# Kernel optimization log

Measured on AMD Instinct MI355X. Metric: run time of the kernel, lower is better.

Reference implementation:

```python
import jax, jax.numpy as jnp
import numpy as np


def hard_sigmoid(x):
    # Keras hard_sigmoid: clip(0.2*x + 0.5, 0, 1)
    return jnp.clip(x * 0.2 + 0.5, 0.0, 1.0)


def conv2d_same(x, w):
    # x: [B,H,W,Cin], w: [kh,kw,Cin,Cout]
    return jax.lax.conv_general_dilated(
        x, w, window_strides=(1, 1), padding='SAME',
        dimension_numbers=('NHWC', 'HWIO', 'NHWC'))


def convlstm2d(x, Wx, Wh, b):
    # x: [B,T,H,W,Cin]; Wx: [k,k,Cin,4*Cout]; Wh: [k,k,Cout,4*Cout]; b: [4*Cout]
    B, T, H, W, _ = x.shape
    Cout = Wh.shape[2]
    h0 = jnp.zeros((B, H, W, Cout), x.dtype)
    c0 = jnp.zeros((B, H, W, Cout), x.dtype)

    def step(carry, xt):
        h, c = carry
        z = conv2d_same(xt, Wx) + conv2d_same(h, Wh) + b
        i, f, g, o = jnp.split(z, 4, axis=-1)  # Keras gate order i,f,c,o
        c = hard_sigmoid(f) * c + hard_sigmoid(i) * jnp.tanh(g)
        h = hard_sigmoid(o) * jnp.tanh(c)
        return (h, c), h

    _, hs = jax.lax.scan(step, (h0, c0), jnp.moveaxis(x, 1, 0))
    return jnp.moveaxis(hs, 0, 1)  # [B,T,H,W,Cout]


def bn_inference(x, gamma, beta, mean, var, eps=1e-3):
    # Keras BatchNormalization default eps=1e-3, inference mode (training=False)
    return (x - mean) * jax.lax.rsqrt(var + eps) * gamma + beta


def upsample_2x2(x):
    # UpSampling3D(size=(1,2,2)) on [B,T,H,W,C]
    return jnp.repeat(jnp.repeat(x, 2, axis=2), 2, axis=3)


def deconv_block(x, Wx, Wh, b, g, be, mm, mv):
    return upsample_2x2(bn_inference(convlstm2d(x, Wx, Wh, b), g, be, mm, mv))


def setup_inputs() -> dict:
    key = jax.random.key(0)
    ks = jax.random.split(key, 32)
    B, T, H, W = 2, 8, 16, 16
    Cin = 192
    chans = [128, 64, 32]
    K = 3
    d = {'x': jax.random.normal(ks[0], (B, T, H, W, Cin), jnp.float32)}
    ci = Cin
    ki = 1
    for l, co in enumerate(chans, start=1):
        d[f'Wx{l}'] = jax.random.normal(ks[ki], (K, K, ci, 4 * co), jnp.float32) * 0.05; ki += 1
        d[f'Wh{l}'] = jax.random.normal(ks[ki], (K, K, co, 4 * co), jnp.float32) * 0.05; ki += 1
        d[f'b{l}'] = jnp.zeros((4 * co,), jnp.float32)
        d[f'g{l}'] = jax.random.uniform(ks[ki], (co,), jnp.float32) + 0.5; ki += 1
        d[f'be{l}'] = jax.random.normal(ks[ki], (co,), jnp.float32) * 0.1; ki += 1
        d[f'mm{l}'] = jax.random.normal(ks[ki], (co,), jnp.float32) * 0.1; ki += 1
        d[f'mv{l}'] = jax.random.uniform(ks[ki], (co,), jnp.float32) + 0.5; ki += 1
        ci = co
    return d


def reference(x, Wx1, Wh1, b1, g1, be1, mm1, mv1,
              Wx2, Wh2, b2, g2, be2, mm2, mv2,
              Wx3, Wh3, b3, g3, be3, mm3, mv3):
    x = deconv_block(x, Wx1, Wh1, b1, g1, be1, mm1, mv1)  # [2,8,32,32,128]
    x = deconv_block(x, Wx2, Wh2, b2, g2, be2, mm2, mv2)  # [2,8,64,64,64]
    x = deconv_block(x, Wx3, Wh3, b3, g3, be3, mm3, mv3)  # [2,8,128,128,32]
    return x
```

## Files before the change

### kernel.cpp

```cpp
#include <hip/hip_runtime.h>
#include <math.h>

#define BATCH 2
#define TSTEPS 8

typedef __attribute__((ext_vector_type(8))) short s16x8;
typedef __attribute__((ext_vector_type(4))) float f32x4;

__device__ __forceinline__ float hsig(float v){ return fminf(fmaxf(0.2f*v+0.5f,0.f),1.f); }
__device__ __forceinline__ ushort f2bf(float f){
    uint u = __builtin_bit_cast(uint, f);
    u = (u + 0x7FFFu + ((u >> 16) & 1u)) >> 16;
    return (ushort)u;
}
__device__ __forceinline__ uint pack2bf(float lo, float hi){
    return (uint)f2bf(lo) | ((uint)f2bf(hi) << 16);
}

template<int KCH, int Co>
__device__ __forceinline__ void packw(const float* __restrict__ W, ushort* __restrict__ dst, int d){
    int j = d & 7, lane = (d >> 3) & 63;
    int q = lane >> 4, l = lane & 15;
    int rest = d >> 9;
    int c = rest % KCH, t_n = rest / KCH;
    int k = c*32 + q*8 + j;
    int np = t_n*16 + l;
    int g = np & 3, co = np >> 2;
    dst[d] = f2bf(W[(size_t)k*(4*Co) + g*Co + co]);
}

#define SZ_X    786432
#define SZ_WX1  884736
#define SZ_WH1  589824
#define SZ_WX2  294912
#define SZ_WH2  147456
#define SZ_WX3  73728
#define SZ_WH3  36864
#define SZ_PREP (SZ_X+SZ_WX1+SZ_WH1+SZ_WX2+SZ_WH2+SZ_WX3+SZ_WH3)

struct Params {
    const float *x, *Wx1, *Wh1, *b1, *g1, *be1, *mm1, *mv1;
    const float *Wx2, *Wh2, *b2, *g2, *be2, *mm2, *mv2;
    const float *Wx3, *Wh3, *b3, *g3, *be3, *mm3, *mv3;
    float *c1, *c2, *c3;
    char  *zbase;
    ushort *xpad, *x2pad, *x3pad, *h1A, *h1B, *h2A, *h2B, *h3A, *h3B;
    ushort *Wxp1, *Wxp2, *Wxp3, *Whp1, *Whp2, *Whp3;
    float *out;
};

__device__ __forceinline__ void prep_elem(int i, const Params& p){
    if (i < SZ_X){
        int c = i % 192; int r = i / 192;
        int xx = r % 16; r /= 16; int yy = r % 16; int bt = r / 16;
        p.xpad[((size_t)bt*18*18 + (yy+1)*18 + (xx+1))*192 + c] = f2bf(p.x[i]);
        return;
    } i -= SZ_X;
    if (i < SZ_WX1){ packw<54,128>(p.Wx1, p.Wxp1, i); return; } i -= SZ_WX1;
    if (i < SZ_WH1){ packw<36,128>(p.Wh1, p.Whp1, i); return; } i -= SZ_WH1;
    if (i < SZ_WX2){ packw<36, 64>(p.Wx2, p.Wxp2, i); return; } i -= SZ_WX2;
    if (i < SZ_WH2){ packw<18, 64>(p.Wh2, p.Whp2, i); return; } i -= SZ_WH2;
    if (i < SZ_WX3){ packw<18, 32>(p.Wx3, p.Wxp3, i); return; } i -= SZ_WX3;
    if (i < SZ_WH3){ packw< 9, 32>(p.Wh3, p.Whp3, i); }
}

__global__ __launch_bounds__(256) void prep_kernel_g(Params p){
    int i = blockIdx.x*256 + threadIdx.x;
    if (i < SZ_PREP) prep_elem(i, p);
}

template<int CI, int CO, int H, int W, int OUT_BF16>
__device__ __forceinline__ void fused_role(char* smem, int lbid, int t, int first,
    const ushort* __restrict__ Apad, const ushort* __restrict__ Wxpk,
    const ushort* __restrict__ hprev, const ushort* __restrict__ Whpk,
    const float* __restrict__ bias,
    ushort* __restrict__ hnew, float* __restrict__ cst,
    const float* __restrict__ gamma, const float* __restrict__ beta,
    const float* __restrict__ mmean, const float* __restrict__ mvar,
    void* __restrict__ outp)
{
    constexpr int W_T = (W < 32) ? W : 32;
    constexpr int PR = (32/W_T) + 2, PPX = W_T + 2;
    constexpr int PCI = CI + 8, PCO = CO + 8;
    constexpr int KX = 9*CI/32, CPTX = CI/32;
    constexpr int KH = 9*CO/32, CPTH = CO/32;
    constexpr int NJX = (KX + 3)/4, NJH = (KH + 3)/4;
    constexpr int HW = H*W, HP = H+2, WP = W+2;
    constexpr int CH8X = CI/8, CH8H = CO/8;
    constexpr int TOTX = PR*PPX*CH8X, TOTH = PR*PPX*CH8H;
    constexpr int PT = (BATCH*HW)/32;

    ushort* patch = (ushort*)smem;
    float* Zs = (float*)smem;
    float* Hs = (float*)(smem + 18432);

    const int tid = threadIdx.x, lane = tid & 63, wave = tid >> 6;
    const int quad = lane >> 4, l16 = lane & 15;
    const int pxt = lbid % PT, colIdx = lbid / PT;
    const int m0 = pxt * 32;
    const int b2 = m0 / HW, rem = m0 - b2*HW;
    const int y0 = rem / W, x0 = rem - (rem/W)*W;
    const int co0 = colIdx * 8;
    const int tn0 = colIdx * 2;
    const int bt = b2*TSTEPS + t;

    f32x4 acc[2][2] = {};

    {
        const ushort* gsrc = Apad + (size_t)bt*HP*WP*CI;
        for (int c = tid; c < TOTX; c += 256){
            int pix = c / CH8X, ch = c - pix*CH8X;
            int prow = pix / PPX, ppx = pix - prow*PPX;
            *(uint4*)&patch[pix*PCI + ch*8] =
                *(const uint4*)(gsrc + ((size_t)(y0+prow)*WP + (x0+ppx))*CI + ch*8);
        }
        __syncthreads();

        const ushort* bp0 = Wxpk + ((size_t)tn0*KX*64 + lane)*8;
        const ushort* bp1 = Wxpk + ((size_t)(tn0+1)*KX*64 + lane)*8;
        int labase[2];
        #pragma unroll
        for (int s = 0; s < 2; ++s){
            int pp = s*16 + l16;
            int rp = pp / W_T, xp = pp - rp*W_T;
            labase[s] = (rp*PPX + xp)*PCI + quad*8;
        }
        const int nj = (KX - wave + 3) >> 2;
        #pragma unroll
        for (int j = 0; j < NJX; ++j){
            if (j < nj){
                const int it = wave + 4*j;
                const int tap = it / CPTX, ci0 = (it - tap*CPTX)*32;
                const int kh = tap/3, kw = tap - (tap/3)*3;
                const int off = (kh*PPX + kw)*PCI + ci0;
                s16x8 b0 = *(const s16x8*)(bp0 + (size_t)it*512);
                s16x8 b1 = *(const s16x8*)(bp1 + (size_t)it*512);
                s16x8 a0 = *(const s16x8*)&patch[labase[0] + off];
                s16x8 a1 = *(const s16x8*)&patch[labase[1] + off];
                acc[0][0] = __builtin_amdgcn_mfma_f32_16x16x32_bf16(a0, b0, acc[0][0], 0,0,0);
                acc[0][1] = __builtin_amdgcn_mfma_f32_16x16x32_bf16(a0, b1, acc[0][1], 0,0,0);
                acc[1][0] = __builtin_amdgcn_mfma_f32_16x16x32_bf16(a1, b0, acc[1][0], 0,0,0);
                acc[1][1] = __builtin_amdgcn_mfma_f32_16x16x32_bf16(a1, b1, acc[1][1], 0,0,0);
            }
        }
        __syncthreads();
    }

    if (!first){
        const ushort* gsrc = hprev + (size_t)b2*HP*WP*CO;
        for (int c = tid; c < TOTH; c += 256){
            int pix = c / CH8H, ch = c - pix*CH8H;
            int prow = pix / PPX, ppx = pix - prow*PPX;
            *(uint4*)&patch[pix*PCO + ch*8] =
                *(const uint4*)(gsrc + ((size_t)(y0+prow)*WP + (x0+ppx))*CO + ch*8);
        }
        __syncthreads();

        const ushort* bp0 = Whpk + ((size_t)tn0*KH*64 + lane)*8;
        const ushort* bp1 = Whpk + ((size_t)(tn0+1)*KH*64 + lane)*8;
        int labase[2];
        #pragma unroll
        for (int s = 0; s < 2; ++s){
            int pp = s*16 + l16;
            int rp = pp / W_T, xp = pp - rp*W_T;
            labase[s] = (rp*PPX + xp)*PCO + quad*8;
        }
        const int nj = (KH - wave + 3) >> 2;
        #pragma unroll
        for (int j = 0; j < NJH; ++j){
            if (j < nj){
                const int it = wave + 4*j;
                const int tap = it / CPTH, ci0 = (it - tap*CPTH)*32;
                const int kh = tap/3, kw = tap - (tap/3)*3;
                const int off = (kh*PPX + kw)*PCO + ci0;
                s16x8 b0 = *(const s16x8*)(bp0 + (size_t)it*512);
                s16x8 b1 = *(const s16x8*)(bp1 + (size_t)it*512);
                s16x8 a0 = *(const s16x8*)&patch[labase[0] + off];
                s16x8 a1 = *(const s16x8*)&patch[labase[1] + off];
                acc[0][0] = __builtin_amdgcn_mfma_f32_16x16x32_bf16(a0, b0, acc[0][0], 0,0,0);
                acc[0][1] = __builtin_amdgcn_mfma_f32_16x16x32_bf16(a0, b1, acc[0][1], 0,0,0);
                acc[1][0] = __builtin_amdgcn_mfma_f32_16x16x32_bf16(a1, b0, acc[1][0], 0,0,0);
                acc[1][1] = __builtin_amdgcn_mfma_f32_16x16x32_bf16(a1, b1, acc[1][1], 0,0,0);
            }
        }
        __syncthreads();
    }

    #pragma unroll
    for (int s = 0; s < 2; ++s)
        #pragma unroll
        for (int nt = 0; nt < 2; ++nt)
            #pragma unroll
            for (int r = 0; r < 4; ++r)
                Zs[(wave*32 + s*16 + quad*4 + r)*36 + nt*16 + l16] = acc[s][nt][r];
    __syncthreads();

    {
        const int px = tid >> 3, coin = tid & 7;
        const int m = m0 + px;
        const int rr = m - b2*HW;
        const int co = co0 + coin;
        float zi = 0.f, zf = 0.f, zg = 0.f, zo = 0.f;
        #pragma unroll
        for (int w = 0; w < 4; ++w){
            const float4 s = *(const float4*)&Zs[(w*32 + px)*36 + coin*4];
            zi += s.x; zf += s.y; zg += s.z; zo += s.w;
        }
        zi += bias[0*CO + co]; zf += bias[1*CO + co];
        zg += bias[2*CO + co]; zo += bias[3*CO + co];
        const float iv = hsig(zi), fv = hsig(zf);
        const float gv = tanhf(zg), ov = hsig(zo);
        const float cold = first ? 0.f : cst[(size_t)m*CO + co];
        const float cn = fv*cold + iv*gv;
        cst[(size_t)m*CO + co] = cn;
        const float h = ov * tanhf(cn);
        const int y = rr / W, x = rr - (rr/W)*W;
        hnew[((size_t)b2*HP*WP + (y+1)*WP + (x+1))*CO + co] = f2bf(h);
        Hs[px*8 + coin] = (h - mmean[co])*rsqrtf(mvar[co]+1e-3f)*gamma[co] + beta[co];
    }
    __syncthreads();

    if (OUT_BF16){
        if (tid < 128){
            const int px = tid >> 2, q = tid & 3;
            const int ypos = q >> 1, xpos = q & 1;
            const int m = m0 + px;
            const int rr = m - b2*HW;
            const int y = rr / W, x = rr - (rr/W)*W;
            const float* hs = &Hs[px*8];
            uint4 v;
            v.x = pack2bf(hs[0], hs[1]); v.y = pack2bf(hs[2], hs[3]);
            v.z = pack2bf(hs[4], hs[5]); v.w = pack2bf(hs[6], hs[7]);
            ushort* o = (ushort*)outp;
            const size_t opix = ((size_t)bt*(2*H+2) + 2*y+1+ypos)*(size_t)(2*W+2) + 2*x+1+xpos;
            *(uint4*)&o[opix*CO + co0] = v;
        }
    } else {
        const int px = tid >> 3, q = (tid >> 1) & 3, half = tid & 1;
        const int ypos = q >> 1, xpos = q & 1;
        const int m = m0 + px;
        const int rr = m - b2*HW;
        const int y = rr / W, x = rr - (rr/W)*W;
        float4 v = *(const float4*)&Hs[px*8 + half*4];
        float* o = (float*)outp;
        const size_t opix = ((size_t)bt*(2*H) + 2*y+ypos)*(size_t)(2*W) + 2*x+xpos;
        *(float4*)&o[opix*CO + co0 + half*4] = v;
    }
}

__global__ __launch_bounds__(256) void mega(Params p, int e1, int e2,
                                            int t1, int t2, int t3)
{
    __shared__ __align__(16) char smem[28800];
    const int bid = blockIdx.x;
    if (bid < e1){
        const ushort* hp = (t1 & 1) ? p.h1B : p.h1A;
        ushort*       hn = (t1 & 1) ? p.h1A : p.h1B;
        fused_role<192,128,16,16,1>(smem, bid, t1, t1==0,
            p.xpad, p.Wxp1, hp, p.Whp1, p.b1, hn, p.c1,
            p.g1, p.be1, p.mm1, p.mv1, p.x2pad);
    } else if (bid < e2){
        const ushort* hp = (t2 & 1) ? p.h2B : p.h2A;
        ushort*       hn = (t2 & 1) ? p.h2A : p.h2B;
        fused_role<128,64,32,32,1>(smem, bid - e1, t2, t2==0,
            p.x2pad, p.Wxp2, hp, p.Whp2, p.b2, hn, p.c2,
            p.g2, p.be2, p.mm2, p.mv2, p.x3pad);
    } else {
        const ushort* hp = (t3 & 1) ? p.h3B : p.h3A;
        ushort*       hn = (t3 & 1) ? p.h3A : p.h3B;
        fused_role<64,32,64,64,0>(smem, bid - e2, t3, t3==0,
            p.x3pad, p.Wxp3, hp, p.Whp3, p.b3, hn, p.c3,
            p.g3, p.be3, p.mm3, p.mv3, p.out);
    }
}

extern "C" void kernel_launch(void* const* d_in, const int* in_sizes, int n_in,
                              void* d_out, int out_size, void* d_ws, size_t ws_size,
                              hipStream_t stream) {
    Params p;
    p.x   = (const float*)d_in[0];
    p.Wx1 = (const float*)d_in[1];  p.Wh1 = (const float*)d_in[2];
    p.b1  = (const float*)d_in[3];  p.g1  = (const float*)d_in[4];
    p.be1 = (const float*)d_in[5];  p.mm1 = (const float*)d_in[6];
    p.mv1 = (const float*)d_in[7];
    p.Wx2 = (const float*)d_in[8];  p.Wh2 = (const float*)d_in[9];
    p.b2  = (const float*)d_in[10]; p.g2  = (const float*)d_in[11];
    p.be2 = (const float*)d_in[12]; p.mm2 = (const float*)d_in[13];
    p.mv2 = (const float*)d_in[14];
    p.Wx3 = (const float*)d_in[15]; p.Wh3 = (const float*)d_in[16];
    p.b3  = (const float*)d_in[17]; p.g3  = (const float*)d_in[18];
    p.be3 = (const float*)d_in[19]; p.mm3 = (const float*)d_in[20];
    p.mv3 = (const float*)d_in[21];

    char* ws = (char*)d_ws;
    size_t off = 0;
    auto alloc = [&](size_t bytes) { char* q = ws + off; off += (bytes + 255) & ~(size_t)255; return q; };

    p.c1  = (float*)alloc(65536ull * 4);
    p.c2  = (float*)alloc(131072ull * 4);
    p.c3  = (float*)alloc(262144ull * 4);

    p.zbase = alloc(17685504ull);
    p.xpad  = (ushort*)p.zbase;
    p.x2pad = p.xpad  + 995328;
    p.x3pad = p.x2pad + 2367488;
    p.h1A   = p.x3pad + 4460544;
    p.h1B   = p.h1A + 82944;
    p.h2A   = p.h1B + 82944;
    p.h2B   = p.h2A + 147968;
    p.h3A   = p.h2B + 147968;
    p.h3B   = p.h3A + 278784;

    p.Wxp1 = (ushort*)alloc(884736ull * 2);
    p.Wxp2 = (ushort*)alloc(294912ull * 2);
    p.Wxp3 = (ushort*)alloc(73728ull * 2);
    p.Whp1 = (ushort*)alloc(589824ull * 2);
    p.Whp2 = (ushort*)alloc(147456ull * 2);
    p.Whp3 = (ushort*)alloc(36864ull * 2);

    p.out = (float*)d_out;

    hipMemsetAsync(p.zbase, 0, 17685504ull, stream);

    prep_kernel_g<<<(SZ_PREP + 255) / 256, 256, 0, stream>>>(p);

    for (int j = 0; j <= 9; ++j){
        const int aS1 = (j <= 7);
        const int aS2 = (j >= 1 && j <= 8);
        const int aS3 = (j >= 2);
        const int e1 = aS1 ? 256 : 0;
        const int e2 = e1 + (aS2 ? 512 : 0);
        const int e3 = e2 + (aS3 ? 1024 : 0);
        const int t1 = aS1 ? j     : 0;
        const int t2 = aS2 ? j - 1 : 0;
        const int t3 = aS3 ? j - 2 : 0;
        mega<<<dim3(e3), 256, 0, stream>>>(p, e1, e2, t1, t2, t3);
    }
}
```

Before: 258.2 us.

## Compute two column blocks per workgroup for layers 2-3, padding K to multiples of four

Layers 2 and 3 now have each workgroup compute two 8-channel output column blocks (NCPB=2). Each A-fragment read from LDS feeds twice as many MFMAs, and the im2col patch load is amortised over twice the output columns, which halves the grid size for those layers. Packed weights are zero-padded along K to a multiple of four so the per-wave guard on the K loop can be dropped. Costs are more accumulator registers, larger shared memory (38912 bytes) and fewer blocks per launch, which could reduce occupancy and parallelism.

```diff
diff --git a/kernel.cpp b/kernel.cpp
--- a/kernel.cpp
+++ b/kernel.cpp
@@ -17,12 +17,13 @@
     return (uint)f2bf(lo) | ((uint)f2bf(hi) << 16);
 }
 
-template<int KCH, int Co>
+template<int KCH, int KCHP, int Co>
 __device__ __forceinline__ void packw(const float* __restrict__ W, ushort* __restrict__ dst, int d){
     int j = d & 7, lane = (d >> 3) & 63;
     int q = lane >> 4, l = lane & 15;
     int rest = d >> 9;
-    int c = rest % KCH, t_n = rest / KCH;
+    int c = rest % KCHP, t_n = rest / KCHP;
+    if (c >= KCH){ dst[d] = 0; return; }
     int k = c*32 + q*8 + j;
     int np = t_n*16 + l;
     int g = np & 3, co = np >> 2;
@@ -30,12 +31,12 @@
 }
 
 #define SZ_X    786432
-#define SZ_WX1  884736
+#define SZ_WX1  917504
 #define SZ_WH1  589824
 #define SZ_WX2  294912
-#define SZ_WH2  147456
-#define SZ_WX3  73728
-#define SZ_WH3  36864
+#define SZ_WH2  163840
+#define SZ_WX3   81920
+#define SZ_WH3   49152
 #define SZ_PREP (SZ_X+SZ_WX1+SZ_WH1+SZ_WX2+SZ_WH2+SZ_WX3+SZ_WH3)
 
 struct Params {
@@ -56,12 +57,12 @@
         p.xpad[((size_t)bt*18*18 + (yy+1)*18 + (xx+1))*192 + c] = f2bf(p.x[i]);
         return;
     } i -= SZ_X;
-    if (i < SZ_WX1){ packw<54,128>(p.Wx1, p.Wxp1, i); return; } i -= SZ_WX1;
-    if (i < SZ_WH1){ packw<36,128>(p.Wh1, p.Whp1, i); return; } i -= SZ_WH1;
-    if (i < SZ_WX2){ packw<36, 64>(p.Wx2, p.Wxp2, i); return; } i -= SZ_WX2;
-    if (i < SZ_WH2){ packw<18, 64>(p.Wh2, p.Whp2, i); return; } i -= SZ_WH2;
-    if (i < SZ_WX3){ packw<18, 32>(p.Wx3, p.Wxp3, i); return; } i -= SZ_WX3;
-    if (i < SZ_WH3){ packw< 9, 32>(p.Wh3, p.Whp3, i); }
+    if (i < SZ_WX1){ packw<54,56,128>(p.Wx1, p.Wxp1, i); return; } i -= SZ_WX1;
+    if (i < SZ_WH1){ packw<36,36,128>(p.Wh1, p.Whp1, i); return; } i -= SZ_WH1;
+    if (i < SZ_WX2){ packw<36,36, 64>(p.Wx2, p.Wxp2, i); return; } i -= SZ_WX2;
+    if (i < SZ_WH2){ packw<18,20, 64>(p.Wh2, p.Whp2, i); return; } i -= SZ_WH2;
+    if (i < SZ_WX3){ packw<18,20, 32>(p.Wx3, p.Wxp3, i); return; } i -= SZ_WX3;
+    if (i < SZ_WH3){ packw< 9,12, 32>(p.Wh3, p.Whp3, i); }
 }
 
 __global__ __launch_bounds__(256) void prep_kernel_g(Params p){
@@ -69,7 +70,7 @@
     if (i < SZ_PREP) prep_elem(i, p);
 }
 
-template<int CI, int CO, int H, int W, int OUT_BF16>
+template<int CI, int CO, int H, int W, int OUT_BF16, int NCPB>
 __device__ __forceinline__ void fused_role(char* smem, int lbid, int t, int first,
     const ushort* __restrict__ Apad, const ushort* __restrict__ Wxpk,
     const ushort* __restrict__ hprev, const ushort* __restrict__ Whpk,
@@ -84,7 +85,8 @@
     constexpr int PCI = CI + 8, PCO = CO + 8;
     constexpr int KX = 9*CI/32, CPTX = CI/32;
     constexpr int KH = 9*CO/32, CPTH = CO/32;
-    constexpr int NJX = (KX + 3)/4, NJH = (KH + 3)/4;
+    constexpr int KXP = (KX + 3) & ~3, KHP = (KH + 3) & ~3;
+    constexpr int NJX = KXP/4, NJH = KHP/4;
     constexpr int HW = H*W, HP = H+2, WP = W+2;
     constexpr int CH8X = CI/8, CH8H = CO/8;
     constexpr int TOTX = PR*PPX*CH8X, TOTH = PR*PPX*CH8H;
@@ -92,19 +94,26 @@
 
     ushort* patch = (ushort*)smem;
     float* Zs = (float*)smem;
-    float* Hs = (float*)(smem + 18432);
+    float* Hs = (float*)(smem + NCPB*18432);
 
     const int tid = threadIdx.x, lane = tid & 63, wave = tid >> 6;
     const int quad = lane >> 4, l16 = lane & 15;
-    const int pxt = lbid % PT, colIdx = lbid / PT;
+    const int pxt = lbid % PT, colB = lbid / PT;
     const int m0 = pxt * 32;
     const int b2 = m0 / HW, rem = m0 - b2*HW;
     const int y0 = rem / W, x0 = rem - (rem/W)*W;
-    const int co0 = colIdx * 8;
-    const int tn0 = colIdx * 2;
     const int bt = b2*TSTEPS + t;
 
-    f32x4 acc[2][2] = {};
+    f32x4 acc[NCPB][2][2] = {};
+
+    int labaseX[2], labaseH[2];
+    #pragma unroll
+    for (int s = 0; s < 2; ++s){
+        int pp = s*16 + l16;
+        int rp = pp / W_T, xp = pp - rp*W_T;
+        labaseX[s] = (rp*PPX + xp)*PCI + quad*8;
+        labaseH[s] = (rp*PPX + xp)*PCO + quad*8;
+    }
 
     {
         const ushort* gsrc = Apad + (size_t)bt*HP*WP*CI;
@@ -116,31 +125,30 @@
         }
         __syncthreads();
 
-        const ushort* bp0 = Wxpk + ((size_t)tn0*KX*64 + lane)*8;
-        const ushort* bp1 = Wxpk + ((size_t)(tn0+1)*KX*64 + lane)*8;
-        int labase[2];
-        #pragma unroll
-        for (int s = 0; s < 2; ++s){
-            int pp = s*16 + l16;
-            int rp = pp / W_T, xp = pp - rp*W_T;
-            labase[s] = (rp*PPX + xp)*PCI + quad*8;
-        }
-        const int nj = (KX - wave + 3) >> 2;
+        const ushort* bp[NCPB][2];
+        #pragma unroll
+        for (int cc = 0; cc < NCPB; ++cc){
+            const int tn = (colB*NCPB + cc)*2;
+            bp[cc][0] = Wxpk + ((size_t)tn*KXP*64 + lane)*8;
+            bp[cc][1] = Wxpk + ((size_t)(tn+1)*KXP*64 + lane)*8;
+        }
         #pragma unroll
         for (int j = 0; j < NJX; ++j){
-            if (j < nj){
-                const int it = wave + 4*j;
-                const int tap = it / CPTX, ci0 = (it - tap*CPTX)*32;
-                const int kh = tap/3, kw = tap - (tap/3)*3;
-                const int off = (kh*PPX + kw)*PCI + ci0;
-                s16x8 b0 = *(const s16x8*)(bp0 + (size_t)it*512);
-                s16x8 b1 = *(const s16x8*)(bp1 + (size_t)it*512);
-                s16x8 a0 = *(const s16x8*)&patch[labase[0] + off];
-                s16x8 a1 = *(const s16x8*)&patch[labase[1] + off];
-                acc[0][0] = __builtin_amdgcn_mfma_f32_16x16x32_bf16(a0, b0, acc[0][0], 0,0,0);
-                acc[0][1] = __builtin_amdgcn_mfma_f32_16x16x32_bf16(a0, b1, acc[0][1], 0,0,0);
-                acc[1][0] = __builtin_amdgcn_mfma_f32_16x16x32_bf16(a1, b0, acc[1][0], 0,0,0);
-                acc[1][1] = __builtin_amdgcn_mfma_f32_16x16x32_bf16(a1, b1, acc[1][1], 0,0,0);
+            const int it = wave + 4*j;
+            const int itA = (it < KX) ? it : 0;
+            const int tap = itA / CPTX, ci0 = (itA - tap*CPTX)*32;
+            const int kh = tap/3, kw = tap - (tap/3)*3;
+            const int off = (kh*PPX + kw)*PCI + ci0;
+            s16x8 a0 = *(const s16x8*)&patch[labaseX[0] + off];
+            s16x8 a1 = *(const s16x8*)&patch[labaseX[1] + off];
+            #pragma unroll
+            for (int cc = 0; cc < NCPB; ++cc){
+                s16x8 b0 = *(const s16x8*)(bp[cc][0] + (size_t)it*512);
+                s16x8 b1 = *(const s16x8*)(bp[cc][1] + (size_t)it*512);
+                acc[cc][0][0] = __builtin_amdgcn_mfma_f32_16x16x32_bf16(a0, b0, acc[cc][0][0], 0,0,0);
+                acc[cc][0][1] = __builtin_amdgcn_mfma_f32_16x16x32_bf16(a0, b1, acc[cc][0][1], 0,0,0);
+                acc[cc][1][0] = __builtin_amdgcn_mfma_f32_16x16x32_bf16(a1, b0, acc[cc][1][0], 0,0,0);
+                acc[cc][1][1] = __builtin_amdgcn_mfma_f32_16x16x32_bf16(a1, b1, acc[cc][1][1], 0,0,0);
             }
         }
         __syncthreads();
@@ -156,54 +164,56 @@
         }
         __syncthreads();
 
-        const ushort* bp0 = Whpk + ((size_t)tn0*KH*64 + lane)*8;
-        const ushort* bp1 = Whpk + ((size_t)(tn0+1)*KH*64 + lane)*8;
-        int labase[2];
-        #pragma unroll
-        for (int s = 0; s < 2; ++s){
-            int pp = s*16 + l16;
-            int rp = pp / W_T, xp = pp - rp*W_T;
-            labase[s] = (rp*PPX + xp)*PCO + quad*8;
-        }
-        const int nj = (KH - wave + 3) >> 2;
+        const ushort* bp[NCPB][2];
+        #pragma unroll
+        for (int cc = 0; cc < NCPB; ++cc){
+            const int tn = (colB*NCPB + cc)*2;
+            bp[cc][0] = Whpk + ((size_t)tn*KHP*64 + lane)*8;
+            bp[cc][1] = Whpk + ((size_t)(tn+1)*KHP*64 + lane)*8;
+        }
         #pragma unroll
         for (int j = 0; j < NJH; ++j){
-            if (j < nj){
-                const int it = wave + 4*j;
-                const int tap = it / CPTH, ci0 = (it - tap*CPTH)*32;
-                const int kh = tap/3, kw = tap - (tap/3)*3;
-                const int off = (kh*PPX + kw)*PCO + ci0;
-                s16x8 b0 = *(const s16x8*)(bp0 + (size_t)it*512);
-                s16x8 b1 = *(const s16x8*)(bp1 + (size_t)it*512);
-                s16x8 a0 = *(const s16x8*)&patch[labase[0] + off];
-                s16x8 a1 = *(const s16x8*)&patch[labase[1] + off];
-                acc[0][0] = __builtin_amdgcn_mfma_f32_16x16x32_bf16(a0, b0, acc[0][0], 0,0,0);
-                acc[0][1] = __builtin_amdgcn_mfma_f32_16x16x32_bf16(a0, b1, acc[0][1], 0,0,0);
-                acc[1][0] = __builtin_amdgcn_mfma_f32_16x16x32_bf16(a1, b0, acc[1][0], 0,0,0);
-                acc[1][1] = __builtin_amdgcn_mfma_f32_16x16x32_bf16(a1, b1, acc[1][1], 0,0,0);
+            const int it = wave + 4*j;
+            const int itA = (it < KH) ? it : 0;
+            const int tap = itA / CPTH, ci0 = (itA - tap*CPTH)*32;
+            const int kh = tap/3, kw = tap - (tap/3)*3;
+            const int off = (kh*PPX + kw)*PCO + ci0;
+            s16x8 a0 = *(const s16x8*)&patch[labaseH[0] + off];
+            s16x8 a1 = *(const s16x8*)&patch[labaseH[1] + off];
+            #pragma unroll
+            for (int cc = 0; cc < NCPB; ++cc){
+                s16x8 b0 = *(const s16x8*)(bp[cc][0] + (size_t)it*512);
+                s16x8 b1 = *(const s16x8*)(bp[cc][1] + (size_t)it*512);
+                acc[cc][0][0] = __builtin_amdgcn_mfma_f32_16x16x32_bf16(a0, b0, acc[cc][0][0], 0,0,0);
+                acc[cc][0][1] = __builtin_amdgcn_mfma_f32_16x16x32_bf16(a0, b1, acc[cc][0][1], 0,0,0);
+                acc[cc][1][0] = __builtin_amdgcn_mfma_f32_16x16x32_bf16(a1, b0, acc[cc][1][0], 0,0,0);
+                acc[cc][1][1] = __builtin_amdgcn_mfma_f32_16x16x32_bf16(a1, b1, acc[cc][1][1], 0,0,0);
             }
         }
         __syncthreads();
     }
 
     #pragma unroll
-    for (int s = 0; s < 2; ++s)
-        #pragma unroll
-        for (int nt = 0; nt < 2; ++nt)
+    for (int cc = 0; cc < NCPB; ++cc)
+        #pragma unroll
+        for (int s = 0; s < 2; ++s)
             #pragma unroll
-            for (int r = 0; r < 4; ++r)
-                Zs[(wave*32 + s*16 + quad*4 + r)*36 + nt*16 + l16] = acc[s][nt][r];
+            for (int nt = 0; nt < 2; ++nt)
+                #pragma unroll
+                for (int r = 0; r < 4; ++r)
+                    Zs[cc*4608 + (wave*32 + s*16 + quad*4 + r)*36 + nt*16 + l16] = acc[cc][s][nt][r];
     __syncthreads();
 
-    {
+    #pragma unroll
+    for (int cc = 0; cc < NCPB; ++cc){
         const int px = tid >> 3, coin = tid & 7;
         const int m = m0 + px;
         const int rr = m - b2*HW;
-        const int co = co0 + coin;
+        const int co = (colB*NCPB + cc)*8 + coin;
         float zi = 0.f, zf = 0.f, zg = 0.f, zo = 0.f;
         #pragma unroll
         for (int w = 0; w < 4; ++w){
-            const float4 s = *(const float4*)&Zs[(w*32 + px)*36 + coin*4];
+            const float4 s = *(const float4*)&Zs[cc*4608 + (w*32 + px)*36 + coin*4];
             zi += s.x; zf += s.y; zg += s.z; zo += s.w;
         }
         zi += bias[0*CO + co]; zf += bias[1*CO + co];
@@ -216,59 +226,63 @@
         const float h = ov * tanhf(cn);
         const int y = rr / W, x = rr - (rr/W)*W;
         hnew[((size_t)b2*HP*WP + (y+1)*WP + (x+1))*CO + co] = f2bf(h);
-        Hs[px*8 + coin] = (h - mmean[co])*rsqrtf(mvar[co]+1e-3f)*gamma[co] + beta[co];
+        Hs[cc*256 + px*8 + coin] = (h - mmean[co])*rsqrtf(mvar[co]+1e-3f)*gamma[co] + beta[co];
     }
     __syncthreads();
 
-    if (OUT_BF16){
-        if (tid < 128){
-            const int px = tid >> 2, q = tid & 3;
+    #pragma unroll
+    for (int cc = 0; cc < NCPB; ++cc){
+        const int co0 = (colB*NCPB + cc)*8;
+        if (OUT_BF16){
+            if (tid < 128){
+                const int px = tid >> 2, q = tid & 3;
+                const int ypos = q >> 1, xpos = q & 1;
+                const int m = m0 + px;
+                const int rr = m - b2*HW;
+                const int y = rr / W, x = rr - (rr/W)*W;
+                const float* hs = &Hs[cc*256 + px*8];
+                uint4 v;
+                v.x = pack2bf(hs[0], hs[1]); v.y = pack2bf(hs[2], hs[3]);
+                v.z = pack2bf(hs[4], hs[5]); v.w = pack2bf(hs[6], hs[7]);
+                ushort* o = (ushort*)outp;
+                const size_t opix = ((size_t)bt*(2*H+2) + 2*y+1+ypos)*(size_t)(2*W+2) + 2*x+1+xpos;
+                *(uint4*)&o[opix*CO + co0] = v;
+            }
+        } else {
+            const int px = tid >> 3, q = (tid >> 1) & 3, half = tid & 1;
             const int ypos = q >> 1, xpos = q & 1;
             const int m = m0 + px;
             const int rr = m - b2*HW;
             const int y = rr / W, x = rr - (rr/W)*W;
-            const float* hs = &Hs[px*8];
-            uint4 v;
-            v.x = pack2bf(hs[0], hs[1]); v.y = pack2bf(hs[2], hs[3]);
-            v.z = pack2bf(hs[4], hs[5]); v.w = pack2bf(hs[6], hs[7]);
-            ushort* o = (ushort*)outp;
-            const size_t opix = ((size_t)bt*(2*H+2) + 2*y+1+ypos)*(size_t)(2*W+2) + 2*x+1+xpos;
-            *(uint4*)&o[opix*CO + co0] = v;
-        }
-    } else {
-        const int px = tid >> 3, q = (tid >> 1) & 3, half = tid & 1;
-        const int ypos = q >> 1, xpos = q & 1;
-        const int m = m0 + px;
-        const int rr = m - b2*HW;
-        const int y = rr / W, x = rr - (rr/W)*W;
-        float4 v = *(const float4*)&Hs[px*8 + half*4];
-        float* o = (float*)outp;
-        const size_t opix = ((size_t)bt*(2*H) + 2*y+ypos)*(size_t)(2*W) + 2*x+xpos;
-        *(float4*)&o[opix*CO + co0 + half*4] = v;
-    }
-}
-
-__global__ __launch_bounds__(256) void mega(Params p, int e1, int e2,
-                                            int t1, int t2, int t3)
+            float4 v = *(const float4*)&Hs[cc*256 + px*8 + half*4];
+            float* o = (float*)outp;
+            const size_t opix = ((size_t)bt*(2*H) + 2*y+ypos)*(size_t)(2*W) + 2*x+xpos;
+            *(float4*)&o[opix*CO + co0 + half*4] = v;
+        }
+    }
+}
+
+__global__ __launch_bounds__(256, 4) void mega(Params p, int e1, int e2,
+                                               int t1, int t2, int t3)
 {
-    __shared__ __align__(16) char smem[28800];
+    __shared__ __align__(16) char smem[38912];
     const int bid = blockIdx.x;
     if (bid < e1){
         const ushort* hp = (t1 & 1) ? p.h1B : p.h1A;
         ushort*       hn = (t1 & 1) ? p.h1A : p.h1B;
-        fused_role<192,128,16,16,1>(smem, bid, t1, t1==0,
+        fused_role<192,128,16,16,1,1>(smem, bid, t1, t1==0,
             p.xpad, p.Wxp1, hp, p.Whp1, p.b1, hn, p.c1,
             p.g1, p.be1, p.mm1, p.mv1, p.x2pad);
     } else if (bid < e2){
         const ushort* hp = (t2 & 1) ? p.h2B : p.h2A;
         ushort*       hn = (t2 & 1) ? p.h2A : p.h2B;
-        fused_role<128,64,32,32,1>(smem, bid - e1, t2, t2==0,
+        fused_role<128,64,32,32,1,2>(smem, bid - e1, t2, t2==0,
             p.x2pad, p.Wxp2, hp, p.Whp2, p.b2, hn, p.c2,
             p.g2, p.be2, p.mm2, p.mv2, p.x3pad);
     } else {
         const ushort* hp = (t3 & 1) ? p.h3B : p.h3A;
         ushort*       hn = (t3 & 1) ? p.h3A : p.h3B;
-        fused_role<64,32,64,64,0>(smem, bid - e2, t3, t3==0,
+        fused_role<64,32,64,64,0,2>(smem, bid - e2, t3, t3==0,
             p.x3pad, p.Wxp3, hp, p.Whp3, p.b3, hn, p.c3,
             p.g3, p.be3, p.mm3, p.mv3, p.out);
     }
@@ -311,12 +325,12 @@
     p.h3A   = p.h2B + 147968;
     p.h3B   = p.h3A + 278784;
 
-    p.Wxp1 = (ushort*)alloc(884736ull * 2);
-    p.Wxp2 = (ushort*)alloc(294912ull * 2);
-    p.Wxp3 = (ushort*)alloc(73728ull * 2);
-    p.Whp1 = (ushort*)alloc(589824ull * 2);
-    p.Whp2 = (ushort*)alloc(147456ull * 2);
-    p.Whp3 = (ushort*)alloc(36864ull * 2);
+    p.Wxp1 = (ushort*)alloc((size_t)SZ_WX1 * 2);
+    p.Wxp2 = (ushort*)alloc((size_t)SZ_WX2 * 2);
+    p.Wxp3 = (ushort*)alloc((size_t)SZ_WX3 * 2);
+    p.Whp1 = (ushort*)alloc((size_t)SZ_WH1 * 2);
+    p.Whp2 = (ushort*)alloc((size_t)SZ_WH2 * 2);
+    p.Whp3 = (ushort*)alloc((size_t)SZ_WH3 * 2);
 
     p.out = (float*)d_out;
 
@@ -329,8 +343,8 @@
         const int aS2 = (j >= 1 && j <= 8);
         const int aS3 = (j >= 2);
         const int e1 = aS1 ? 256 : 0;
-        const int e2 = e1 + (aS2 ? 512 : 0);
-        const int e3 = e2 + (aS3 ? 1024 : 0);
+        const int e2 = e1 + (aS2 ? 256 : 0);
+        const int e3 = e2 + (aS3 ? 512 : 0);
         const int t1 = aS1 ? j     : 0;
         const int t2 = aS2 ? j - 1 : 0;
         const int t3 = aS3 ? j - 2 : 0;
```

After: 257.2 us. Within noise of the previous version (-0.4%).
